# Optimization experiments

Hardware: AMD Instinct MI355X
Metric: run time of the kernel (lower is better)

The kernel has to match this reference:

```python
import jax
jax.config.update("jax_enable_x64", True)
import jax.numpy as jnp
import numpy as np

SIGMA_2 = 0.1  # SNR = 10 dB -> sigma^2 = 1/10^(10/10)
P = 1.0        # total transmit power

NT, NR, DK, KU, BR = 64, 4, 2, 8, 16
BATCH = 256


def setup_inputs() -> dict:
    key = jax.random.key(0)
    k1, k2 = jax.random.split(key)
    channel = jax.random.normal(k1, (BATCH, NT * NR * BR * 2 * KU), dtype=jnp.float32)
    pred_w = 2 * NR * DK * KU * BR + DK * DK * KU * BR  # 2560
    prediction = jax.random.normal(k2, (BATCH, pred_w), dtype=jnp.float32)
    return {"channel": channel, "prediction": prediction,
            "Nt": NT, "Nr": NR, "dk": DK, "K": KU, "B": BR}


def reference(channel, prediction, Nt, Nr, dk, K, B):
    # --- unpack complex channel: [b, Nt, Nr, B, 2K] -> [b, Nr, Nt, B, K] complex
    Hc = channel.reshape(-1, Nt, Nr, B, 2 * K).astype(jnp.complex128)
    H = Hc[..., :K] + 1j * Hc[..., K:]
    H = jnp.transpose(H, (0, 2, 1, 3, 4))  # [b, Nr, Nt, B, K]

    nu = 2 * Nr * dk * K * B
    u_flat = prediction[:, :nu]
    w_flat = prediction[:, nu:nu + dk * dk * K * B]
    Uc = u_flat.reshape(-1, Nr, dk, B, 2 * K).astype(jnp.complex128)
    U = Uc[..., :K] + 1j * Uc[..., K:]           # [b, Nr, dk, B, K]
    W = w_flat.reshape(-1, dk, dk, B, K).astype(jnp.complex128)  # real-valued W

    # HHU[b,:,:,f,k] = H^H U  -> [b, Nt, dk, B, K]
    HHU = jnp.einsum('brtfk,brdfk->btdfk', jnp.conj(H), U)

    # sum over (rb, user) of sigma2/p * trace(U W U^H)
    tr_UWU = (SIGMA_2 / P) * jnp.einsum('brdfk,bdefk,brefk->b', U, W, jnp.conj(U))
    # sum over (rb, user) of (H^H U) W (H^H U)^H  -> [b, Nt, Nt]
    quad = jnp.einsum('btdfk,bdefk,bsefk->bts', HHU, W, jnp.conj(HHU))
    temp_B = quad + tr_UWU[:, None, None] * jnp.eye(Nt, dtype=jnp.complex128)
    temp_B_inv = jnp.linalg.inv(temp_B)  # batched Nt x Nt complex inverse

    # HUW[b,:,:,k] = sum_rb (H^H U) W  -> [b, Nt, dk, K]
    HUW = jnp.einsum('btdfk,bdefk->btek', HHU, W)
    V0 = jnp.einsum('bts,bsdk->btdk', temp_B_inv, HUW)  # [b, Nt, dk, K]

    # l2-normalize flattened precoder per sample (tf.linalg.normalize)
    flat = V0.reshape(-1, Nt * dk * K)
    flat = flat / jnp.linalg.norm(flat, axis=1, keepdims=True)
    V0 = flat.reshape(-1, Nt, dk, K)

    # power normalization: trace(sum_k V_k V_k^H)
    trace_VV = jnp.einsum('btdk,btdk->b', V0, jnp.conj(V0))
    scale = jnp.sqrt(P / jnp.real(trace_VV).astype(jnp.float32))
    V = V0 * scale.astype(jnp.complex128)[:, None, None, None]

    V = V.reshape(-1, Nt, dk, K, 1)
    return jnp.concatenate([jnp.real(V), jnp.imag(V)], axis=4).astype(jnp.float32)
```

## Files before the change

### kernel.cpp

```cpp
#include <hip/hip_runtime.h>
#include <math.h>


#define SAUG 84
#define STP  65

namespace {
union alignas(16) ShU {
    struct { float4 TtP[2][2][8][STP]; float4 HtP[2][2][8][STP]; } p1;
    float2 Aug[64][SAUG];
};
struct alignas(16) ShV {
    float2 U[4 * 258];
    float  W[512];
};
}

__device__ __forceinline__ float2 cmul(float2 x, float2 y) {
    return make_float2(x.x * y.x - x.y * y.y, x.x * y.y + x.y * y.x);
}

__global__ __launch_bounds__(512, 1)
void uw2v_build(const float* __restrict__ channel,
                const float* __restrict__ prediction,
                float2* __restrict__ wsAug,
                float2* __restrict__ wsTr)
{
    __shared__ ShU sh;
    __shared__ ShV sv;
    __shared__ float2 redbuf[8];

    const int bid = blockIdx.x;
    const int b   = bid >> 1;
    const int hf  = bid & 1;
    const int tid = threadIdx.x;
    const int wv  = tid >> 6;
    const float* pred = prediction + (size_t)b * 2560;
    const float* chan = channel + (size_t)b * 65536;

    #pragma unroll
    for (int i = 0; i < 2; ++i) {
        int m = tid + i * 512;
        int r = m >> 8, d = (m >> 7) & 1, f = (m >> 3) & 15, k = m & 7;
        const float* src = pred + (((r * 2 + d) * 16 + f) << 4);
        sv.U[r * 258 + ((d * 16 + f) << 3) + k] = make_float2(src[k], src[k + 8]);
    }
    sv.W[tid] = pred[2048 + tid];
    __syncthreads();

    const int grp2 = tid >> 8;
    const int lt   = tid & 255;
    const int t4 = lt >> 2, r4 = lt & 3;
    const int a  = lt >> 4, bb = lt & 15;
    const int bit0 = r4 & 1, bit1 = (r4 >> 1) & 1;
    const int kkb  = 4 * bit0 + 2 * bit1;
    const int mpb  = kkb >> 1;
    const int fbase = ((hf << 1) | grp2) << 2;
    const int tr_r = lt >> 5, tr_d = (lt >> 4) & 1, tr_e = (lt >> 3) & 1, tr_k = lt & 7;

    float2 accA[4][4], accB[4][4];
    #pragma unroll
    for (int i = 0; i < 4; ++i)
        #pragma unroll
        for (int j = 0; j < 4; ++j) {
            accA[i][j] = make_float2(0.f, 0.f);
            accB[i][j] = make_float2(0.f, 0.f);
        }
    float2 huw[4] = {make_float2(0,0), make_float2(0,0), make_float2(0,0), make_float2(0,0)};
    float2 tracc  = make_float2(0.f, 0.f);

    const float* hbase = chan + ((t4 * 4 + r4) << 8) + (fbase << 4);

    #pragma unroll 1
    for (int fi = 0; fi < 4; ++fi) {
        const int f = fbase + fi;
        const float4 ca = *(const float4*)(hbase + (fi << 4) + 0);
        const float4 cb = *(const float4*)(hbase + (fi << 4) + 4);
        const float4 ci = *(const float4*)(hbase + (fi << 4) + 8);
        const float4 cd = *(const float4*)(hbase + (fi << 4) + 12);

        const float4* U0p = (const float4*)&sv.U[r4 * 258 + (f << 3)];
        const float4* U1p = (const float4*)&sv.U[r4 * 258 + ((16 + f) << 3)];
        const float4 u0q0 = U0p[0], u0q1 = U0p[1], u0q2 = U0p[2], u0q3 = U0p[3];
        const float4 u1q0 = U1p[0], u1q1 = U1p[1], u1q2 = U1p[2], u1q3 = U1p[3];

        float2 val0[8], val1[8];
        #define MK2(K, HR, HI, U0R, U0I, U1R, U1I) \
            val0[K] = make_float2((HR)*(U0R) + (HI)*(U0I), (HR)*(U0I) - (HI)*(U0R)); \
            val1[K] = make_float2((HR)*(U1R) + (HI)*(U1I), (HR)*(U1I) - (HI)*(U1R));
        MK2(0, ca.x, ci.x, u0q0.x, u0q0.y, u1q0.x, u1q0.y)
        MK2(1, ca.y, ci.y, u0q0.z, u0q0.w, u1q0.z, u1q0.w)
        MK2(2, ca.z, ci.z, u0q1.x, u0q1.y, u1q1.x, u1q1.y)
        MK2(3, ca.w, ci.w, u0q1.z, u0q1.w, u1q1.z, u1q1.w)
        MK2(4, cb.x, cd.x, u0q2.x, u0q2.y, u1q2.x, u1q2.y)
        MK2(5, cb.y, cd.y, u0q2.z, u0q2.w, u1q2.z, u1q2.w)
        MK2(6, cb.z, cd.z, u0q3.x, u0q3.y, u1q3.x, u1q3.y)
        MK2(7, cb.w, cd.w, u0q3.z, u0q3.w, u1q3.z, u1q3.w)
        #undef MK2

        float2 s1d0[4], s1d1[4];
        #pragma unroll
        for (int q = 0; q < 4; ++q) {
            float2 k0 = bit0 ? val0[4 + q] : val0[q];
            float2 n0 = bit0 ? val0[q]     : val0[4 + q];
            float2 k1 = bit0 ? val1[4 + q] : val1[q];
            float2 n1 = bit0 ? val1[q]     : val1[4 + q];
            n0.x = __shfl_xor(n0.x, 1); n0.y = __shfl_xor(n0.y, 1);
            n1.x = __shfl_xor(n1.x, 1); n1.y = __shfl_xor(n1.y, 1);
            s1d0[q] = make_float2(k0.x + n0.x, k0.y + n0.y);
            s1d1[q] = make_float2(k1.x + n1.x, k1.y + n1.y);
        }
        float2 h0[2], h1[2];
        #pragma unroll
        for (int jj = 0; jj < 2; ++jj) {
            float2 k0 = bit1 ? s1d0[2 + jj] : s1d0[jj];
            float2 n0 = bit1 ? s1d0[jj]     : s1d0[2 + jj];
            float2 k1 = bit1 ? s1d1[2 + jj] : s1d1[jj];
            float2 n1 = bit1 ? s1d1[jj]     : s1d1[2 + jj];
            n0.x = __shfl_xor(n0.x, 2); n0.y = __shfl_xor(n0.y, 2);
            n1.x = __shfl_xor(n1.x, 2); n1.y = __shfl_xor(n1.y, 2);
            h0[jj] = make_float2(k0.x + n0.x, k0.y + n0.y);
            h1[jj] = make_float2(k1.x + n1.x, k1.y + n1.y);
        }

        if (lt < 128) {
            float w   = sv.W[((tr_d * 2 + tr_e) * 16 + f) * 8 + tr_k];
            float2 u1 = sv.U[tr_r * 258 + ((tr_d * 16 + f) << 3) + tr_k];
            float2 u2 = sv.U[tr_r * 258 + ((tr_e * 16 + f) << 3) + tr_k];
            tracc.x += w * (u1.x * u2.x + u1.y * u2.y);
            tracc.y += w * (u1.y * u2.x - u1.x * u2.y);
        }

        const int p = fi & 1;
        #pragma unroll
        for (int e = 0; e < 2; ++e) {
            float w0a = sv.W[(e * 16 + f) * 8 + kkb];
            float w0b = sv.W[(e * 16 + f) * 8 + kkb + 1];
            float w1a = sv.W[((2 + e) * 16 + f) * 8 + kkb];
            float w1b = sv.W[((2 + e) * 16 + f) * 8 + kkb + 1];
            float2 tva = make_float2(h0[0].x * w0a + h1[0].x * w1a,
                                     h0[0].y * w0a + h1[0].y * w1a);
            float2 tvb = make_float2(h0[1].x * w0b + h1[1].x * w1b,
                                     h0[1].y * w0b + h1[1].y * w1b);
            sh.p1.TtP[p][grp2][e * 4 + mpb][t4] = make_float4(tva.x, tva.y, tvb.x, tvb.y);
            huw[e * 2 + 0].x += tva.x; huw[e * 2 + 0].y += tva.y;
            huw[e * 2 + 1].x += tvb.x; huw[e * 2 + 1].y += tvb.y;
        }
        sh.p1.HtP[p][grp2][mpb][t4]     = make_float4(h0[0].x, h0[0].y, h0[1].x, h0[1].y);
        sh.p1.HtP[p][grp2][4 + mpb][t4] = make_float4(h1[0].x, h1[0].y, h1[1].x, h1[1].y);
        __syncthreads();

        #pragma unroll
        for (int mp = 0; mp < 8; ++mp) {
            float4 tq[4], hq[4];
            #pragma unroll
            for (int i = 0; i < 4; ++i) tq[i] = sh.p1.TtP[p][grp2][mp][a + 16 * i];
            #pragma unroll
            for (int j = 0; j < 4; ++j) hq[j] = sh.p1.HtP[p][grp2][mp][bb + 16 * j];
            #pragma unroll
            for (int i = 0; i < 4; ++i)
                #pragma unroll
                for (int j = 0; j < 4; ++j) {
                    float2 va = accA[i][j], vb = accB[i][j];
                    va.x = fmaf(tq[i].x, hq[j].x, va.x);
                    va.y = fmaf(tq[i].x, hq[j].y, va.y);
                    vb.x = fmaf(tq[i].y, hq[j].x, vb.x);
                    vb.y = fmaf(tq[i].y, hq[j].y, vb.y);
                    va.x = fmaf(tq[i].z, hq[j].z, va.x);
                    va.y = fmaf(tq[i].z, hq[j].w, va.y);
                    vb.x = fmaf(tq[i].w, hq[j].z, vb.x);
                    vb.y = fmaf(tq[i].w, hq[j].w, vb.y);
                    accA[i][j] = va; accB[i][j] = vb;
                }
        }
    }

    #pragma unroll
    for (int off = 32; off; off >>= 1) {
        tracc.x += __shfl_xor(tracc.x, off);
        tracc.y += __shfl_xor(tracc.y, off);
    }
    if ((tid & 63) == 0) redbuf[wv] = tracc;
    __syncthreads();
    if (tid == 0) {
        float2 s = make_float2(0.f, 0.f);
        #pragma unroll
        for (int w = 0; w < 8; ++w) { s.x += redbuf[w].x; s.y += redbuf[w].y; }
        wsTr[bid] = s;
    }

    if (grp2 == 0) {
        #pragma unroll
        for (int i = 0; i < 4; ++i)
            #pragma unroll
            for (int j = 0; j < 4; ++j)
                sh.Aug[a + 16 * i][bb + 16 * j] =
                    make_float2(accA[i][j].x + accB[i][j].y,
                                accB[i][j].x - accA[i][j].y);
        #pragma unroll
        for (int e = 0; e < 2; ++e)
            #pragma unroll
            for (int jj = 0; jj < 2; ++jj)
                sh.Aug[t4][64 + e * 8 + kkb + jj] = huw[e * 2 + jj];
    }
    __syncthreads();
    if (grp2 == 1) {
        #pragma unroll
        for (int i = 0; i < 4; ++i)
            #pragma unroll
            for (int j = 0; j < 4; ++j) {
                float2 v = sh.Aug[a + 16 * i][bb + 16 * j];
                v.x += accA[i][j].x + accB[i][j].y;
                v.y += accB[i][j].x - accA[i][j].y;
                sh.Aug[a + 16 * i][bb + 16 * j] = v;
            }
        #pragma unroll
        for (int e = 0; e < 2; ++e)
            #pragma unroll
            for (int jj = 0; jj < 2; ++jj) {
                int col = 64 + e * 8 + kkb + jj;
                float2 v = sh.Aug[t4][col];
                v.x += huw[e * 2 + jj].x; v.y += huw[e * 2 + jj].y;
                sh.Aug[t4][col] = v;
            }
    }
    __syncthreads();

    {
        const int row = tid >> 3, q = tid & 7;
        const float4* src = (const float4*)&sh.Aug[row][q * 10];
        float4* dst = (float4*)(wsAug + (size_t)bid * 5120 + row * 80 + q * 10);
        #pragma unroll
        for (int j = 0; j < 5; ++j) dst[j] = src[j];
    }
}

__global__ __launch_bounds__(1024)
void uw2v_gj(const float2* __restrict__ wsAug,
             const float2* __restrict__ wsTr,
             float2* __restrict__ out)
{
    __shared__ alignas(16) float2 prow[2][80];
    __shared__ float2 xout[64][17];
    __shared__ float  fred[16];

    const int b   = blockIdx.x;
    const int tid = threadIdx.x;
    const int wv  = tid >> 6;

    const float2 tA = wsTr[2 * b], tB = wsTr[2 * b + 1];
    const float2 trv = make_float2((tA.x + tB.x) * 0.1f, (tA.y + tB.y) * 0.1f);

    const int gi = tid >> 4, gc = tid & 15;
    const int cb = gc * 5;
    const int lanebase = (tid & 63) & 48;

    const float2* A0 = wsAug + (size_t)(2 * b) * 5120 + gi * 80;
    const float2* A1 = wsAug + (size_t)(2 * b + 1) * 5120 + gi * 80;

    float2 xr[5];
    #pragma unroll
    for (int c = 0; c < 5; ++c) {
        float2 v = A0[cb + c];
        float2 w = A1[cb + c];
        v.x += w.x; v.y += w.y;
        if (gi == cb + c) { v.x += trv.x; v.y += trv.y; }
        xr[c] = v;
    }
    if (gi == 0) {
        #pragma unroll
        for (int c = 0; c < 5; ++c) prow[0][cb + c] = xr[c];
    }
    __syncthreads();

    float2 myipv = make_float2(0.f, 0.f);

    #pragma unroll 1
    for (int ks = 0; ks < 64; ++ks) {
        const int pb = ks & 1;
        float2 pr[5];
        #pragma unroll
        for (int c = 0; c < 5; ++c) pr[c] = prow[pb][cb + c];

        float2 z = prow[pb][ks];
        float  zi = 1.0f / (z.x * z.x + z.y * z.y);
        float2 ipv = make_float2(z.x * zi, -z.y * zi);

        float2 cand = make_float2(0.f, 0.f);
        #pragma unroll
        for (int c = 0; c < 5; ++c)
            if (cb + c == ks) cand = xr[c];
        int srcl = lanebase + (ks / 5);
        float2 Lv;
        Lv.x = __shfl(cand.x, srcl);
        Lv.y = __shfl(cand.y, srcl);

        if (gi == ks) {
            myipv = ipv;
        } else {
            float2 L = cmul(Lv, ipv);
            #pragma unroll
            for (int c = 0; c < 5; ++c) {
                xr[c].x -= L.x * pr[c].x - L.y * pr[c].y;
                xr[c].y -= L.x * pr[c].y + L.y * pr[c].x;
            }
        }
        if (gi == ks + 1) {
            #pragma unroll
            for (int c = 0; c < 5; ++c) prow[pb ^ 1][cb + c] = xr[c];
        }
        __syncthreads();
    }

    float ss = 0.f;
    if (gc >= 12) {
        #pragma unroll
        for (int c = 0; c < 5; ++c) {
            int col = cb + c;
            if (col >= 64) {
                float2 xv = cmul(xr[c], myipv);
                ss += xv.x * xv.x + xv.y * xv.y;
                xout[gi][col - 64] = xv;
            }
        }
    }
    #pragma unroll
    for (int off = 32; off; off >>= 1) ss += __shfl_xor(ss, off);
    if ((tid & 63) == 0) fred[wv] = ss;
    __syncthreads();
    float total = 0.f;
    #pragma unroll
    for (int w = 0; w < 16; ++w) total += fred[w];
    float invn = rsqrtf(total);
    {
        float2 v = xout[tid >> 4][tid & 15];
        out[(size_t)b * 1024 + tid] = make_float2(v.x * invn, v.y * invn);
    }
}

extern "C" void kernel_launch(void* const* d_in, const int* in_sizes, int n_in,
                              void* d_out, int out_size, void* d_ws, size_t ws_size,
                              hipStream_t stream) {
    const float* channel    = (const float*)d_in[0];
    const float* prediction = (const float*)d_in[1];
    int batch = in_sizes[0] / 65536;
    float2* wsAug = (float2*)d_ws;
    float2* wsTr  = wsAug + (size_t)batch * 2 * 5120;
    uw2v_build<<<dim3(batch * 2), dim3(512), 0, stream>>>(channel, prediction,
                                                          wsAug, wsTr);
    uw2v_gj<<<dim3(batch), dim3(1024), 0, stream>>>(wsAug, wsTr, (float2*)d_out);
}
```

Measured before the change: 183.9 us.

## Block Gauss-Jordan elimination into 4-row panels to cut barriers

The Gauss-Jordan solve now eliminates four pivot rows per step instead of one. The wavefront that owns each 4-row panel factors it among its own lanes using shuffles, then publishes the pivot rows and inverse pivots to shared memory for the other wavefronts. This cuts the barriers in the solve from 64 to about 16, at the cost of serialising the panel cascade inside one wave while the other waves eliminate. The build kernel also drops double-buffering of its shared TtP/HtP tiles in favour of a second barrier per iteration, and shrinks the Aug padding.

```diff
diff --git a/kernel.cpp b/kernel.cpp
--- a/kernel.cpp
+++ b/kernel.cpp
@@ -2,12 +2,12 @@
 #include <math.h>
 
 
-#define SAUG 84
+#define SAUG 82
 #define STP  65
 
 namespace {
 union alignas(16) ShU {
-    struct { float4 TtP[2][2][8][STP]; float4 HtP[2][2][8][STP]; } p1;
+    struct { float4 TtP[2][8][STP]; float4 HtP[2][8][STP]; } p1;
     float2 Aug[64][SAUG];
 };
 struct alignas(16) ShV {
@@ -131,7 +131,6 @@
             tracc.y += w * (u1.y * u2.x - u1.x * u2.y);
         }
 
-        const int p = fi & 1;
         #pragma unroll
         for (int e = 0; e < 2; ++e) {
             float w0a = sv.W[(e * 16 + f) * 8 + kkb];
@@ -142,21 +141,21 @@
                                      h0[0].y * w0a + h1[0].y * w1a);
             float2 tvb = make_float2(h0[1].x * w0b + h1[1].x * w1b,
                                      h0[1].y * w0b + h1[1].y * w1b);
-            sh.p1.TtP[p][grp2][e * 4 + mpb][t4] = make_float4(tva.x, tva.y, tvb.x, tvb.y);
+            sh.p1.TtP[grp2][e * 4 + mpb][t4] = make_float4(tva.x, tva.y, tvb.x, tvb.y);
             huw[e * 2 + 0].x += tva.x; huw[e * 2 + 0].y += tva.y;
             huw[e * 2 + 1].x += tvb.x; huw[e * 2 + 1].y += tvb.y;
         }
-        sh.p1.HtP[p][grp2][mpb][t4]     = make_float4(h0[0].x, h0[0].y, h0[1].x, h0[1].y);
-        sh.p1.HtP[p][grp2][4 + mpb][t4] = make_float4(h1[0].x, h1[0].y, h1[1].x, h1[1].y);
+        sh.p1.HtP[grp2][mpb][t4]     = make_float4(h0[0].x, h0[0].y, h0[1].x, h0[1].y);
+        sh.p1.HtP[grp2][4 + mpb][t4] = make_float4(h1[0].x, h1[0].y, h1[1].x, h1[1].y);
         __syncthreads();
 
         #pragma unroll
         for (int mp = 0; mp < 8; ++mp) {
             float4 tq[4], hq[4];
             #pragma unroll
-            for (int i = 0; i < 4; ++i) tq[i] = sh.p1.TtP[p][grp2][mp][a + 16 * i];
-            #pragma unroll
-            for (int j = 0; j < 4; ++j) hq[j] = sh.p1.HtP[p][grp2][mp][bb + 16 * j];
+            for (int i = 0; i < 4; ++i) tq[i] = sh.p1.TtP[grp2][mp][a + 16 * i];
+            #pragma unroll
+            for (int j = 0; j < 4; ++j) hq[j] = sh.p1.HtP[grp2][mp][bb + 16 * j];
             #pragma unroll
             for (int i = 0; i < 4; ++i)
                 #pragma unroll
@@ -173,6 +172,7 @@
                     accA[i][j] = va; accB[i][j] = vb;
                 }
         }
+        __syncthreads();
     }
 
     #pragma unroll
@@ -240,7 +240,8 @@
              const float2* __restrict__ wsTr,
              float2* __restrict__ out)
 {
-    __shared__ alignas(16) float2 prow[2][80];
+    __shared__ alignas(16) float2 pivR[2][4][80];
+    __shared__ float2 pivI[2][4];
     __shared__ float2 xout[64][17];
     __shared__ float  fred[16];
 
@@ -267,49 +268,87 @@
         if (gi == cb + c) { v.x += trv.x; v.y += trv.y; }
         xr[c] = v;
     }
-    if (gi == 0) {
-        #pragma unroll
-        for (int c = 0; c < 5; ++c) prow[0][cb + c] = xr[c];
-    }
-    __syncthreads();
 
     float2 myipv = make_float2(0.f, 0.f);
 
+    auto cascade = [&](int chunk, int nb) {
+        #pragma unroll
+        for (int p = 0; p < 4; ++p) {
+            const int col = 4 * chunk + p;
+            const int cs  = col / 5;
+            float2 zc = make_float2(0.f, 0.f);
+            #pragma unroll
+            for (int c = 0; c < 5; ++c)
+                if (cb + c == col) zc = xr[c];
+            float2 z;
+            z.x = __shfl(zc.x, p * 16 + cs);
+            z.y = __shfl(zc.y, p * 16 + cs);
+            float  zi  = 1.0f / (z.x * z.x + z.y * z.y);
+            float2 ipv = make_float2(z.x * zi, -z.y * zi);
+            const bool isPiv = (gi == col);
+            if (isPiv) myipv = ipv;
+            float2 cand = make_float2(0.f, 0.f);
+            #pragma unroll
+            for (int c = 0; c < 5; ++c)
+                if (cb + c == col) cand = xr[c];
+            float2 Lv;
+            Lv.x = __shfl(cand.x, lanebase + cs);
+            Lv.y = __shfl(cand.y, lanebase + cs);
+            float2 pr[5];
+            #pragma unroll
+            for (int c = 0; c < 5; ++c) {
+                pr[c].x = __shfl(xr[c].x, p * 16 + gc);
+                pr[c].y = __shfl(xr[c].y, p * 16 + gc);
+            }
+            if (!isPiv) {
+                float2 L = cmul(Lv, ipv);
+                #pragma unroll
+                for (int c = 0; c < 5; ++c) {
+                    xr[c].x -= L.x * pr[c].x - L.y * pr[c].y;
+                    xr[c].y -= L.x * pr[c].y + L.y * pr[c].x;
+                }
+            }
+        }
+        const int prw = gi - 4 * chunk;
+        #pragma unroll
+        for (int c = 0; c < 5; ++c) pivR[nb][prw][cb + c] = xr[c];
+        if (gc == 0) pivI[nb][prw] = myipv;
+    };
+
+    auto eliminate = [&](int chunk, int bf) {
+        #pragma unroll
+        for (int p = 0; p < 4; ++p) {
+            const int col = 4 * chunk + p;
+            float2 cand = make_float2(0.f, 0.f);
+            #pragma unroll
+            for (int c = 0; c < 5; ++c)
+                if (cb + c == col) cand = xr[c];
+            float2 Lv;
+            Lv.x = __shfl(cand.x, lanebase + col / 5);
+            Lv.y = __shfl(cand.y, lanebase + col / 5);
+            float2 ipv = pivI[bf][p];
+            float2 L = cmul(Lv, ipv);
+            #pragma unroll
+            for (int c = 0; c < 5; ++c) {
+                float2 pr = pivR[bf][p][cb + c];
+                xr[c].x -= L.x * pr.x - L.y * pr.y;
+                xr[c].y -= L.x * pr.y + L.y * pr.x;
+            }
+        }
+    };
+
+    int cur = 0;
+    if (wv == 0) cascade(0, 0);
+    __syncthreads();
+
     #pragma unroll 1
-    for (int ks = 0; ks < 64; ++ks) {
-        const int pb = ks & 1;
-        float2 pr[5];
-        #pragma unroll
-        for (int c = 0; c < 5; ++c) pr[c] = prow[pb][cb + c];
-
-        float2 z = prow[pb][ks];
-        float  zi = 1.0f / (z.x * z.x + z.y * z.y);
-        float2 ipv = make_float2(z.x * zi, -z.y * zi);
-
-        float2 cand = make_float2(0.f, 0.f);
-        #pragma unroll
-        for (int c = 0; c < 5; ++c)
-            if (cb + c == ks) cand = xr[c];
-        int srcl = lanebase + (ks / 5);
-        float2 Lv;
-        Lv.x = __shfl(cand.x, srcl);
-        Lv.y = __shfl(cand.y, srcl);
-
-        if (gi == ks) {
-            myipv = ipv;
-        } else {
-            float2 L = cmul(Lv, ipv);
-            #pragma unroll
-            for (int c = 0; c < 5; ++c) {
-                xr[c].x -= L.x * pr[c].x - L.y * pr[c].y;
-                xr[c].y -= L.x * pr[c].y + L.y * pr[c].x;
-            }
-        }
-        if (gi == ks + 1) {
-            #pragma unroll
-            for (int c = 0; c < 5; ++c) prow[pb ^ 1][cb + c] = xr[c];
+    for (int c = 0; c < 16; ++c) {
+        if (wv != c) {
+            eliminate(c, cur);
+            if (wv == c + 1) cascade(c + 1, cur ^ 1);
         }
         __syncthreads();
+        cur ^= 1;
     }
 
     float ss = 0.f;
```

New measurement: 180.1 us. 2.0% less time.
